# Kernel tuning notes

Measured on AMD Instinct MI355X. Metric: run time of the kernel, lower is better.

The kernel has to match this reference:

```python
import jax, jax.numpy as jnp
import numpy as np

Q_HEADS = 16
KV_HEADS = 4
ROPE_THETA = 10000.0


def _rope(x, seq_len):
    # x: [B, S, H, D]; pairs are consecutive along D (view_as_complex semantics)
    D = x.shape[-1]
    inv_freq = 1.0 / (ROPE_THETA ** (jnp.arange(0, D, 2, dtype=jnp.float32) / D))
    freqs = jnp.arange(seq_len, dtype=jnp.float32)[:, None] * inv_freq  # [S, D/2]
    cos = jnp.cos(freqs)[None, :, None, :]
    sin = jnp.sin(freqs)[None, :, None, :]
    xr = x.reshape(x.shape[:-1] + (D // 2, 2))
    x0, x1 = xr[..., 0], xr[..., 1]
    out = jnp.stack([x0 * cos - x1 * sin, x0 * sin + x1 * cos], axis=-1)
    return out.reshape(x.shape)


def setup_inputs() -> dict:
    key = jax.random.key(0)
    ks = jax.random.split(key, 6)
    B, S, E = 1, 2048, 2048
    KV_DIM = KV_HEADS * (E // Q_HEADS)  # 512
    scale = 0.02
    return {
        "x": jax.random.normal(ks[0], (B, S, E), dtype=jnp.float32),
        "Wq": jax.random.normal(ks[1], (E, E), dtype=jnp.float32) * scale,
        "Wk": jax.random.normal(ks[2], (KV_DIM, E), dtype=jnp.float32) * scale,
        "Wv": jax.random.normal(ks[3], (KV_DIM, E), dtype=jnp.float32) * scale,
        "Wo": jax.random.normal(ks[4], (E, E), dtype=jnp.float32) * scale,
        "bo": jax.random.normal(ks[5], (E,), dtype=jnp.float32) * scale,
        "cache_keys": jnp.zeros((B, S, KV_HEADS, E // Q_HEADS), dtype=jnp.float32),
        "cache_value": jnp.zeros((B, S, KV_HEADS, E // Q_HEADS), dtype=jnp.float32),
        "start_pos": 0,
    }


def reference(x, Wq, Wk, Wv, Wo, bo, cache_keys, cache_value, start_pos):
    B, S, E = x.shape
    hd = E // Q_HEADS
    G = Q_HEADS // KV_HEADS  # queries per kv head

    xq = (x @ Wq.T).reshape(B, S, Q_HEADS, hd)
    xk = (x @ Wk.T).reshape(B, S, KV_HEADS, hd)
    xv = (x @ Wv.T).reshape(B, S, KV_HEADS, hd)

    # Original applies RoPE with positions 0..seq_len-1 for both q and k
    # (freq tensor is sliced [:seq_len] inside apply_rotry_position_embedding).
    xq = _rope(xq, S)
    xk = _rope(xk, S)

    # cache write at start_pos (static python int)
    cache_keys = jax.lax.dynamic_update_slice(cache_keys, xk, (0, start_pos, 0, 0))
    cache_value = jax.lax.dynamic_update_slice(cache_value, xv, (0, start_pos, 0, 0))
    total = start_pos + S
    k_full = cache_keys[:, :total]   # [B, T, KVH, hd]
    v_full = cache_value[:, :total]

    # repeat_interleave over the head axis == GQA expansion
    k = jnp.repeat(k_full, G, axis=2)  # [B, T, QH, hd]
    v = jnp.repeat(v_full, G, axis=2)

    scores = jnp.einsum("bshd,bthd->bhst", xq, k) / jnp.sqrt(jnp.float32(hd))
    causal = jnp.triu(jnp.ones((S, total), dtype=bool), k=1)  # [S, T]
    scores = jnp.where(causal[None, None, :, :], -jnp.inf, scores)
    weights = jax.nn.softmax(scores, axis=-1)
    out = jnp.einsum("bhst,bthd->bshd", weights, v).reshape(B, S, E)
    # dropout p=0.0 / eval mode -> identity
    return out @ Wo.T + bo
```

## Files before the change

### kernel.cpp

```cpp
#include <hip/hip_runtime.h>
#include <stdint.h>

typedef unsigned short u16;
typedef float  f32x4  __attribute__((ext_vector_type(4)));
typedef float  f32x16 __attribute__((ext_vector_type(16)));
typedef __bf16 bf16x8 __attribute__((ext_vector_type(8)));
typedef __bf16 bf16x4 __attribute__((ext_vector_type(4)));
typedef unsigned short u16x8 __attribute__((ext_vector_type(8)));
typedef unsigned short u16x4v __attribute__((ext_vector_type(4)));
typedef unsigned int u32x2 __attribute__((ext_vector_type(2)));
typedef unsigned int u32x4 __attribute__((ext_vector_type(4)));

#define S_LEN 2048
#define E_DIM 2048
#define HD    128
#define QH    16
#define KVH   4
#define KVD   512
#define NQKV  3072
#define QK_SCALE 0.08838834764831845f

#define AS1 __attribute__((address_space(1)))
#define AS3 __attribute__((address_space(3)))

__device__ __forceinline__ u16 f2bf(float f) {
  union { float f; uint32_t u; } v; v.f = f;
  return (u16)((v.u + 0x7FFFu + ((v.u >> 16) & 1u)) >> 16);
}

__global__ void cast_all_kernel(const float* __restrict__ x, const float* __restrict__ Wq,
                                const float* __restrict__ Wk, const float* __restrict__ Wv,
                                const float* __restrict__ Wo,
                                u16* __restrict__ xb, u16* __restrict__ Wcat,
                                u16* __restrict__ Wob, float2* __restrict__ tab) {
  int i = blockIdx.x * blockDim.x + threadIdx.x;
  if (i >= 3670016) {
    int j = i - 3670016;
    int s = j >> 6, pidx = j & 63;
    float inv = exp2f((float)pidx * (-13.287712379549449f / 64.0f));
    float sn, cs;
    sincosf((float)s * inv, &sn, &cs);
    tab[j] = make_float2(cs, sn);
    return;
  }
  const float* src; u16* dst;
  if (i < (1 << 20))                       { src = x  + (size_t)i * 4;  dst = xb + (size_t)i * 4; }
  else if (i < (2 << 20))                  { size_t j = i - (1 << 20);  src = Wq + j * 4; dst = Wcat + j * 4; }
  else if (i < (2 << 20) + (1 << 18))      { size_t j = i - (2 << 20);  src = Wk + j * 4; dst = Wcat + (size_t)E_DIM * E_DIM + j * 4; }
  else if (i < (2 << 20) + (2 << 18))      { size_t j = i - (2 << 20) - (1 << 18); src = Wv + j * 4; dst = Wcat + (size_t)(E_DIM + KVD) * E_DIM + j * 4; }
  else                                     { size_t j = i - (2 << 20) - (2 << 18); src = Wo + j * 4; dst = Wob + j * 4; }
  float4 f = *reinterpret_cast<const float4*>(src);
  u16x4v o;
  o[0] = f2bf(f.x); o[1] = f2bf(f.y); o[2] = f2bf(f.z); o[3] = f2bf(f.w);
  *reinterpret_cast<u16x4v*>(dst) = o;
}

template<bool BIAS, int MODE>
__global__ __launch_bounds__(256) void gemm_bt_kernel(
    const u16* __restrict__ A, const u16* __restrict__ B,
    float* __restrict__ C, const float* __restrict__ bias,
    const float2* __restrict__ tab, u16* __restrict__ qb,
    u16* __restrict__ kb, u16* __restrict__ vTp,
    int M, int N, int K)
{
  __shared__ u16 As[2][64 * 64];
  __shared__ u16 Bs[2][128 * 64];

  const int tid  = threadIdx.x;
  const int lane = tid & 63;
  const int wid  = tid >> 6;
  const int wc   = wid * 32;
  const int lr   = lane & 15;
  const int kg   = lane >> 4;
  const int sw   = lr & 7;

  const int bm = blockIdx.y * 64;
  const int bn = blockIdx.x * 128;

  f32x4 acc[4][2];
  #pragma unroll
  for (int r = 0; r < 4; ++r)
    #pragma unroll
    for (int c = 0; c < 2; ++c) acc[r][c] = (f32x4){0.f, 0.f, 0.f, 0.f};

  const int srow   = wid * 8 + (lane >> 3);
  const int schunk = (lane & 7) ^ (lane >> 3);

  const u16* gA = A + (size_t)(bm + srow) * K + schunk * 8;
  const u16* gB = B + (size_t)(bn + srow) * K + schunk * 8;

  auto stage = [&](int buf, int kt) {
    #pragma unroll
    for (int i = 0; i < 2; ++i)
      __builtin_amdgcn_global_load_lds(
          (const AS1 void*)(gA + (size_t)i * 32 * K + kt),
          (AS3 void*)(&As[buf][(wid*8 + i*32) * 64]), 16, 0, 0);
    #pragma unroll
    for (int i = 0; i < 4; ++i)
      __builtin_amdgcn_global_load_lds(
          (const AS1 void*)(gB + (size_t)i * 32 * K + kt),
          (AS3 void*)(&Bs[buf][(wid*8 + i*32) * 64]), 16, 0, 0);
  };

  stage(0, 0);
  __syncthreads();

  int cur = 0;
  for (int kt = 0; kt < K; kt += 64) {
    if (kt + 64 < K) stage(cur ^ 1, kt + 64);
    #pragma unroll
    for (int kk = 0; kk < 2; ++kk) {
      bf16x8 af[4], bfr[2];
      #pragma unroll
      for (int r = 0; r < 4; ++r)
        af[r] = *reinterpret_cast<const bf16x8*>(
            &As[cur][(r*16 + lr)*64 + ((kk*4 + kg) ^ sw)*8]);
      #pragma unroll
      for (int c = 0; c < 2; ++c)
        bfr[c] = *reinterpret_cast<const bf16x8*>(
            &Bs[cur][(wc + c*16 + lr)*64 + ((kk*4 + kg) ^ sw)*8]);
      #pragma unroll
      for (int r = 0; r < 4; ++r)
        #pragma unroll
        for (int c = 0; c < 2; ++c)
          acc[r][c] = __builtin_amdgcn_mfma_f32_16x16x32_bf16(af[r], bfr[c], acc[r][c], 0, 0, 0);
    }
    __syncthreads();
    cur ^= 1;
  }

  const int crow = kg * 4;
  #pragma unroll
  for (int r = 0; r < 4; ++r) {
    #pragma unroll
    for (int c = 0; c < 2; ++c) {
      int gr = bm + r*16 + crow;
      int gc = bn + wc + c*16 + lr;
      if constexpr (MODE == 0) {
        float badd = BIAS ? bias[gc] : 0.0f;
        #pragma unroll
        for (int reg = 0; reg < 4; ++reg)
          C[(size_t)(gr + reg)*N + gc] = acc[r][c][reg] + badd;
      } else {
        if (gc < E_DIM + KVD) {
          int pidx = (gc & 127) >> 1;
          bool odd = lr & 1;
          #pragma unroll
          for (int reg = 0; reg < 4; ++reg) {
            float val = acc[r][c][reg];
            float oth = __shfl_xor(val, 1);
            float2 cs = tab[(gr + reg) * 64 + pidx];
            float o = odd ? (oth * cs.y + val * cs.x)
                          : (val * cs.x - oth * cs.y);
            if (gc < E_DIM)
              qb[(size_t)(gr + reg) * E_DIM + gc] = f2bf(o * QK_SCALE);
            else
              kb[(size_t)(gr + reg) * KVD + (gc - E_DIM)] = f2bf(o);
          }
        } else {
          bf16x4 pk;
          #pragma unroll
          for (int reg = 0; reg < 4; ++reg) pk[reg] = (__bf16)acc[r][c][reg];
          *reinterpret_cast<bf16x4*>(
              &vTp[(size_t)(gc - E_DIM - KVD) * S_LEN + gr]) = pk;
        }
      }
    }
  }
}

__global__ __launch_bounds__(256, 2) void attn_kernel(
    const u16* __restrict__ Q, const u16* __restrict__ Kc,
    const u16* __restrict__ VT, u16* __restrict__ Out)
{
  __shared__ u16 Ks[2][64 * 128];
  __shared__ u16 VTs[2][128 * 64];

  const int x = blockIdx.x;
  int qt, h;
  if (x < 256) { qt = x & 31; h = x >> 5; }
  else         { int xp = x - 256; qt = 31 - (xp & 31); h = 8 + (xp >> 5); }
  const int kvh = h >> 2;
  const int tid  = threadIdx.x;
  const int lane = tid & 63;
  const int wid  = tid >> 6;
  const int kvg  = wid & 1;
  const int rowg = wid >> 1;
  const int ln   = lane & 31;
  const int hi   = lane >> 5;

  const int NT = qt + 1;

  bf16x8 qf[8];
  {
    const u16* qa = Q + (size_t)(qt*64 + rowg*32 + ln) * E_DIM + h * HD + hi * 8;
    #pragma unroll
    for (int ks = 0; ks < 8; ++ks)
      qf[ks] = *reinterpret_cast<const bf16x8*>(qa + ks * 16);
  }

  f32x16 o4[4];
  #pragma unroll
  for (int d = 0; d < 4; ++d)
    #pragma unroll
    for (int r = 0; r < 16; ++r) o4[d][r] = 0.f;
  float mr = -1e30f, ls = 0.f;

  u16x8 kreg[4], vreg[4];
  const u16* kbase = Kc + kvh * HD;
  const u16* vbase = VT + (size_t)(kvh * HD) * S_LEN;

  auto stage_load = [&](int t) {
    #pragma unroll
    for (int i = 0; i < 4; ++i) {
      int c = i * 256 + tid;
      kreg[i] = *reinterpret_cast<const u16x8*>(
          kbase + (size_t)(t*64 + (c >> 4)) * KVD + (c & 15) * 8);
      vreg[i] = *reinterpret_cast<const u16x8*>(
          vbase + (size_t)(c >> 3) * S_LEN + t*64 + (c & 7) * 8);
    }
  };
  auto stage_write = [&](int b) {
    #pragma unroll
    for (int i = 0; i < 4; ++i) {
      int c = i * 256 + tid;
      int kr = c >> 4, kc = c & 15;
      *reinterpret_cast<u16x8*>(&Ks[b][kr*128 + (kc ^ (kr & 7))*8]) = kreg[i];
      int vr = c >> 3, vc = c & 7;
      *reinterpret_cast<u16x8*>(&VTs[b][vr*64 + (vc ^ (vr & 7))*8]) = vreg[i];
    }
  };

  int p = 0;
  stage_load(0);
  stage_write(0);
  __syncthreads();

  const int krow = kvg*32 + ln;

  for (int t = 0; t < NT; ++t) {
    if (t + 1 < NT) stage_load(t + 1);

    f32x16 st;
    #pragma unroll
    for (int r = 0; r < 16; ++r) st[r] = 0.f;
    __builtin_amdgcn_s_setprio(1);
    #pragma unroll
    for (int ks = 0; ks < 8; ++ks) {
      bf16x8 kfr = *reinterpret_cast<const bf16x8*>(
          &Ks[p][krow*128 + ((ks*2 + hi) ^ (ln & 7))*8]);
      st = __builtin_amdgcn_mfma_f32_32x32x16_bf16(kfr, qf[ks], st, 0, 0, 0);
    }
    __builtin_amdgcn_s_setprio(0);

    if (t == qt) {
      #pragma unroll
      for (int reg = 0; reg < 16; ++reg) {
        int kvl = kvg*32 + 4*hi + (reg & 3) + 8*(reg >> 2);
        if (kvl > rowg*32 + ln) st[reg] = -1e30f;
      }
    }

    float pm = -1e30f;
    #pragma unroll
    for (int reg = 0; reg < 16; ++reg) pm = fmaxf(pm, st[reg]);
    pm = fmaxf(pm, __shfl_xor(pm, 32));

    if (!__all(pm - mr <= 8.0f)) {
      float nm = fmaxf(mr, pm);
      float alpha = __expf(mr - nm);
      ls *= alpha;
      mr = nm;
      #pragma unroll
      for (int reg = 0; reg < 16; ++reg) {
        int crow = (reg & 3) + 8*(reg >> 2) + 4*hi;
        float ar = __shfl(alpha, crow);
        #pragma unroll
        for (int d = 0; d < 4; ++d) o4[d][reg] *= ar;
      }
    }

    float pv[16];
    float sum = 0.f;
    #pragma unroll
    for (int reg = 0; reg < 16; ++reg) {
      pv[reg] = __expf(st[reg] - mr);
      sum += pv[reg];
    }
    sum += __shfl_xor(sum, 32);
    ls += sum;

    bf16x8 pa[2];
    #pragma unroll
    for (int ks = 0; ks < 2; ++ks) {
      bf16x4 A4, B4;
      #pragma unroll
      for (int j = 0; j < 4; ++j) {
        A4[j] = (__bf16)pv[ks*8 + j];
        B4[j] = (__bf16)pv[ks*8 + 4 + j];
      }
      u32x2 uA = __builtin_bit_cast(u32x2, A4);
      u32x2 uB = __builtin_bit_cast(u32x2, B4);
      unsigned sx = hi ? uA[0] : uB[0];
      unsigned sy = hi ? uA[1] : uB[1];
      unsigned rx = __shfl_xor(sx, 32);
      unsigned ry = __shfl_xor(sy, 32);
      u32x4 w;
      w[0] = hi ? rx : uA[0];
      w[1] = hi ? ry : uA[1];
      w[2] = hi ? uB[0] : rx;
      w[3] = hi ? uB[1] : ry;
      pa[ks] = __builtin_bit_cast(bf16x8, w);
    }

    __builtin_amdgcn_s_setprio(1);
    #pragma unroll
    for (int d = 0; d < 4; ++d) {
      int vrow = d*32 + ln;
      #pragma unroll
      for (int ks = 0; ks < 2; ++ks) {
        bf16x8 vb = *reinterpret_cast<const bf16x8*>(
            &VTs[p][vrow*64 + ((kvg*4 + ks*2 + hi) ^ (ln & 7))*8]);
        o4[d] = __builtin_amdgcn_mfma_f32_32x32x16_bf16(pa[ks], vb, o4[d], 0, 0, 0);
      }
    }
    __builtin_amdgcn_s_setprio(0);

    if (t + 1 < NT) {
      stage_write(p ^ 1);
      __syncthreads();
      p ^= 1;
    }
  }

  __syncthreads();
  float* Obuf = (float*)&Ks[0][0];
  float* Lbuf = (float*)&VTs[0][0];
  if (kvg == 1) {
    if (hi == 0) { Lbuf[rowg*32 + ln] = mr; Lbuf[64 + rowg*32 + ln] = ls; }
    #pragma unroll
    for (int reg = 0; reg < 16; ++reg) {
      int crow = (reg & 3) + 8*(reg >> 2) + 4*hi;
      #pragma unroll
      for (int d = 0; d < 4; ++d)
        Obuf[(rowg*32 + crow)*128 + d*32 + ln] = o4[d][reg];
    }
  }
  __syncthreads();
  if (kvg == 0) {
    float mB = Lbuf[rowg*32 + ln];
    float lB = Lbuf[64 + rowg*32 + ln];
    float m  = fmaxf(mr, mB);
    float a0 = __expf(mr - m);
    float a1 = __expf(mB - m);
    float inv = 1.0f / (ls*a0 + lB*a1);
    #pragma unroll
    for (int reg = 0; reg < 16; ++reg) {
      int crow = (reg & 3) + 8*(reg >> 2) + 4*hi;
      float a0r = __shfl(a0, crow);
      float a1r = __shfl(a1, crow);
      float ivr = __shfl(inv, crow);
      int grow = qt*64 + rowg*32 + crow;
      #pragma unroll
      for (int d = 0; d < 4; ++d) {
        float v = (o4[d][reg]*a0r +
                   Obuf[(rowg*32 + crow)*128 + d*32 + ln]*a1r) * ivr;
        Out[(size_t)grow * E_DIM + h * HD + d*32 + ln] =
            __builtin_bit_cast(u16, (__bf16)v);
      }
    }
  }
}

extern "C" void kernel_launch(void* const* d_in, const int* in_sizes, int n_in,
                              void* d_out, int out_size, void* d_ws, size_t ws_size,
                              hipStream_t stream)
{
  const float* x  = (const float*)d_in[0];
  const float* Wq = (const float*)d_in[1];
  const float* Wk = (const float*)d_in[2];
  const float* Wv = (const float*)d_in[3];
  const float* Wo = (const float*)d_in[4];
  const float* bo = (const float*)d_in[5];
  float* out = (float*)d_out;

  char* w = (char*)d_ws;
  u16*    xb   = (u16*)(w);
  u16*    Wcat = (u16*)(w + (8u  << 20));
  u16*    Wob  = (u16*)(w + (20u << 20));
  float2* tab  = (float2*)(w + (28u << 20));
  u16*    qb   = (u16*)(w + (30u << 20));
  u16*    kb   = (u16*)(w + (38u << 20));
  u16*    vT   = (u16*)(w + (40u << 20));
  u16*    attn = (u16*)(w + (42u << 20));
  (void)ws_size; (void)in_sizes; (void)n_in; (void)out_size;

  cast_all_kernel<<<14848, 256, 0, stream>>>(x, Wq, Wk, Wv, Wo, xb, Wcat, Wob, tab);

  gemm_bt_kernel<false, 2><<<dim3(NQKV/128, S_LEN/64), 256, 0, stream>>>(
      xb, Wcat, nullptr, nullptr, tab, qb, kb, vT, S_LEN, NQKV, E_DIM);

  attn_kernel<<<512, 256, 0, stream>>>(qb, kb, vT, attn);

  gemm_bt_kernel<true, 0><<<dim3(E_DIM/128, S_LEN/64), 256, 0, stream>>>(
      attn, Wob, out, bo, nullptr, nullptr, nullptr, nullptr, S_LEN, E_DIM, E_DIM);
}
```

Measured before the change: 130.1 us.

## Load K tiles via direct global-to-LDS DMA and single-buffer V in attention

```diff
diff --git a/kernel.cpp b/kernel.cpp
--- a/kernel.cpp
+++ b/kernel.cpp
@@ -174,7 +174,7 @@
     const u16* __restrict__ VT, u16* __restrict__ Out)
 {
   __shared__ u16 Ks[2][64 * 128];
-  __shared__ u16 VTs[2][128 * 64];
+  __shared__ u16 VTs[128 * 64];
 
   const int x = blockIdx.x;
   int qt, h;
@@ -206,40 +206,51 @@
     for (int r = 0; r < 16; ++r) o4[d][r] = 0.f;
   float mr = -1e30f, ls = 0.f;
 
-  u16x8 kreg[4], vreg[4];
   const u16* kbase = Kc + kvh * HD;
   const u16* vbase = VT + (size_t)(kvh * HD) * S_LEN;
 
-  auto stage_load = [&](int t) {
+  const int kr_off = lane >> 4;
+  const int kchunk = lane & 15;
+  auto k_dma = [&](int buf, int t) {
+    #pragma unroll
+    for (int j = 0; j < 4; ++j) {
+      int r0 = j*16 + wid*4;
+      int r  = r0 + kr_off;
+      const u16* src = kbase + (size_t)(t*64 + r) * KVD + ((kchunk ^ (r & 7)) * 8);
+      __builtin_amdgcn_global_load_lds((const AS1 void*)src,
+          (AS3 void*)(&Ks[buf][r0 * 128]), 16, 0, 0);
+    }
+  };
+
+  u16x8 vreg[4];
+  auto v_load = [&](int t) {
     #pragma unroll
     for (int i = 0; i < 4; ++i) {
       int c = i * 256 + tid;
-      kreg[i] = *reinterpret_cast<const u16x8*>(
-          kbase + (size_t)(t*64 + (c >> 4)) * KVD + (c & 15) * 8);
       vreg[i] = *reinterpret_cast<const u16x8*>(
           vbase + (size_t)(c >> 3) * S_LEN + t*64 + (c & 7) * 8);
     }
   };
-  auto stage_write = [&](int b) {
+  auto v_write = [&]() {
     #pragma unroll
     for (int i = 0; i < 4; ++i) {
       int c = i * 256 + tid;
-      int kr = c >> 4, kc = c & 15;
-      *reinterpret_cast<u16x8*>(&Ks[b][kr*128 + (kc ^ (kr & 7))*8]) = kreg[i];
-      int vr = c >> 3, vc = c & 7;
-      *reinterpret_cast<u16x8*>(&VTs[b][vr*64 + (vc ^ (vr & 7))*8]) = vreg[i];
+      int d = c >> 3;
+      *reinterpret_cast<u16x8*>(&VTs[d*64 + ((c & 7) ^ (d & 7)) * 8]) = vreg[i];
     }
   };
 
+  k_dma(0, 0);
+  v_load(0);
+  v_write();
+  __syncthreads();
+
+  const int krow = kvg*32 + ln;
+
   int p = 0;
-  stage_load(0);
-  stage_write(0);
-  __syncthreads();
-
-  const int krow = kvg*32 + ln;
-
   for (int t = 0; t < NT; ++t) {
-    if (t + 1 < NT) stage_load(t + 1);
+    const bool lastt = (t + 1 == NT);
+    if (!lastt) { k_dma(p ^ 1, t + 1); v_load(t + 1); }
 
     f32x16 st;
     #pragma unroll
@@ -320,14 +331,15 @@
       #pragma unroll
       for (int ks = 0; ks < 2; ++ks) {
         bf16x8 vb = *reinterpret_cast<const bf16x8*>(
-            &VTs[p][vrow*64 + ((kvg*4 + ks*2 + hi) ^ (ln & 7))*8]);
+            &VTs[vrow*64 + ((kvg*4 + ks*2 + hi) ^ (ln & 7))*8]);
         o4[d] = __builtin_amdgcn_mfma_f32_32x32x16_bf16(pa[ks], vb, o4[d], 0, 0, 0);
       }
     }
     __builtin_amdgcn_s_setprio(0);
 
-    if (t + 1 < NT) {
-      stage_write(p ^ 1);
+    if (!lastt) {
+      __syncthreads();
+      v_write();
       __syncthreads();
       p ^= 1;
     }
@@ -335,7 +347,7 @@
 
   __syncthreads();
   float* Obuf = (float*)&Ks[0][0];
-  float* Lbuf = (float*)&VTs[0][0];
+  float* Lbuf = (float*)&VTs[0];
   if (kvg == 1) {
     if (hi == 0) { Lbuf[rowg*32 + ln] = mr; Lbuf[64 + rowg*32 + ln] = ls; }
     #pragma unroll
```

Result: slower. 139.4 us (+7.2%).
